# Kernel tuning notes

Hardware: AMD Instinct MI355X
Metric: run time of the kernel (lower is better)

Reference implementation:

```python
import jax, jax.numpy as jnp
import numpy as np

NUM_CLASSES = 3
NUM_ANCHORS = 3
K = 5 + NUM_CLASSES  # box(4) + obj(1) + classes


def _scale_losses(pred, boxes, labels, pos, neg):
    # pred: [B, A*K, H, W] -> [B, A*H*W, K] matching torch view/permute/view
    B, C, H, W = pred.shape
    p = pred.reshape(B, NUM_ANCHORS, K, H, W).transpose(0, 1, 3, 4, 2).reshape(B, -1, K)
    loc, obj, cls = p[..., :4], p[..., 4], p[..., 5:]
    posf = pos.astype(p.dtype)
    # BCE-with-logits, target = pos_mask: softplus(x) - t*x
    loss_obj = jnp.logaddexp(0.0, obj) - obj * posf  # [B, N]
    num_pos = pos.sum(axis=1)                         # [B] int
    num_neg = jnp.minimum(3 * num_pos, neg.sum(axis=1))
    # hard negative mining: take top-num_neg objectness losses among negatives
    masked = jnp.where(neg, loss_obj, -jnp.inf)
    order = jnp.argsort(-masked, axis=1)
    rank = jnp.argsort(order, axis=1)                 # rank 0 = largest neg loss
    sel = neg & (rank < num_neg[:, None])
    obj_per = (jnp.sum(loss_obj * posf, axis=1) +
               jnp.sum(jnp.where(sel, loss_obj, 0.0), axis=1)) / jnp.maximum(1, num_pos)
    # classification CE, mean over positive anchors
    logp = jax.nn.log_softmax(cls, axis=-1)
    ce = -jnp.take_along_axis(logp, labels[..., None].astype(jnp.int32), axis=-1)[..., 0]
    has_pos = num_pos > 0
    denom = jnp.maximum(num_pos, 1).astype(p.dtype)
    cls_per = jnp.where(has_pos, jnp.sum(ce * posf, axis=1) / denom, 0.0)
    # smooth L1 (beta=1), mean over positive anchors x 4 coords
    d = loc - boxes
    ad = jnp.abs(d)
    sl1 = jnp.where(ad < 1.0, 0.5 * d * d, ad - 0.5)
    loc_per = jnp.where(has_pos,
                        jnp.sum(sl1 * posf[..., None], axis=(1, 2)) / (denom * 4.0), 0.0)
    return obj_per.sum(), cls_per.sum(), loc_per.sum()


def _masks(key, shape):
    u = jax.random.uniform(key, shape)
    pos = u < 0.01
    neg = (~pos) & (u < 0.96)
    return pos, neg


def setup_inputs() -> dict:
    key = jax.random.key(0)
    ks = jax.random.split(key, 12)
    B = 128
    grids = [(80, 80), (40, 40), (20, 20)]
    inp = {}
    for i, (H, W) in enumerate(grids):
        N = NUM_ANCHORS * H * W
        inp[f'pred{i}'] = jax.random.normal(ks[4 * i], (B, NUM_ANCHORS * K, H, W), jnp.float32)
        inp[f'boxes{i}'] = jax.random.uniform(ks[4 * i + 1], (B, N, 4), jnp.float32)
        inp[f'labels{i}'] = jax.random.randint(ks[4 * i + 2], (B, N), 0, NUM_CLASSES, jnp.int32)
        pos, neg = _masks(ks[4 * i + 3], (B, N))
        inp[f'pos{i}'] = pos
        inp[f'neg{i}'] = neg
    return inp


def reference(pred0, pred1, pred2, boxes0, boxes1, boxes2,
              labels0, labels1, labels2, pos0, pos1, pos2, neg0, neg1, neg2):
    B = pred0.shape[0]
    preds = (pred0, pred1, pred2)
    boxes = (boxes0, boxes1, boxes2)
    labels = (labels0, labels1, labels2)
    pos = (pos0, pos1, pos2)
    neg = (neg0, neg1, neg2)
    tot_obj = tot_cls = tot_loc = 0.0
    for s in range(3):
        o, c, l = _scale_losses(preds[s], boxes[s], labels[s], pos[s], neg[s])
        tot_obj = tot_obj + o
        tot_cls = tot_cls + c
        tot_loc = tot_loc + l
    loss_obj = tot_obj / B
    loss_cls = tot_cls / B
    loss_loc = tot_loc / B
    return loss_obj + loss_cls + loss_loc, loss_obj, loss_cls, loss_loc
```

## Files before the change

kernel.cpp:

```cpp
#include <hip/hip_runtime.h>
#include <stdint.h>

#define NA   3
#define KCH  8
#define BLK  512
#define NWV  (BLK / 64)
#define NB   2048
#define QCAP 512
#define CCAP 4096
#define LKEY 0xBFA8u

#define LOG2E 1.4426950408889634f
#define LN2   0.6931471805599453f

struct ScaleParams {
  const float*   pred;
  const float*   boxes;
  const int*     labels;
  const uint8_t* pos;
  const uint8_t* neg;
  int HW;
};

__device__ __forceinline__ float fexp2(float x) { return __builtin_amdgcn_exp2f(x); }
__device__ __forceinline__ float flog2(float x) { return __builtin_amdgcn_logf(x); }

__device__ __forceinline__ float softplus_fast(float x) {
  const float t = fexp2(-fabsf(x) * LOG2E);
  return fmaxf(x, 0.f) + flog2(1.f + t) * LN2;
}

__device__ __forceinline__ float sl1f(float d) {
  float ad = fabsf(d);
  return (ad < 1.f) ? 0.5f * d * d : ad - 0.5f;
}

__device__ __forceinline__ unsigned fkey(unsigned u) {
  return (u & 0x80000000u) ? ~u : (u | 0x80000000u);
}
__device__ __forceinline__ unsigned funkey(unsigned k) {
  return (k & 0x80000000u) ? (k & 0x7FFFFFFFu) : ~k;
}
__device__ __forceinline__ float sp16(unsigned k16) {
  return softplus_fast(__uint_as_float(funkey((k16 << 16) | 0x8000u)));
}

struct __align__(16) RowShared {
  unsigned short compact[CCAP];
  unsigned hc[NB];
  float    hs[NB];
  int      queue[QCAP];
  int      sh_qn, sh_nc;
  int      iwav[NWV];
  float    fwav[NWV];
  float    fscr[NWV];
  float    wred[NWV][4];
  int      sh_dig, sh_krem;
  float    sh_sa, sh_avg;
  int      sh_flag;
  unsigned c32[32];
  float    s32[32];
};

__device__ __forceinline__ float blockSum(float v, float* scr) {
  #pragma unroll
  for (int off = 32; off > 0; off >>= 1) v += __shfl_down(v, off);
  const int lane = threadIdx.x & 63, w = threadIdx.x >> 6;
  __syncthreads();
  if (lane == 0) scr[w] = v;
  __syncthreads();
  float r = 0.f;
  #pragma unroll
  for (int i = 0; i < NWV; ++i) r += scr[i];
  return r;
}

__device__ __forceinline__ void selectDigit4(const unsigned* cb, const float* sb,
                                             int krem_in, RowShared& S) {
  const int t = threadIdx.x, lane = t & 63, w = t >> 6;
  int c_t = 0; float s_t = 0.f;
  #pragma unroll
  for (int q = 0; q < 4; ++q) { c_t += (int)cb[q]; s_t += sb[q]; }
  int ci = c_t; float si = s_t;
  #pragma unroll
  for (int off = 1; off < 64; off <<= 1) {
    const int   co = __shfl_down(ci, off);
    const float so = __shfl_down(si, off);
    if (lane + off < 64) { ci += co; si += so; }
  }
  __syncthreads();
  if (lane == 0) { S.iwav[w] = ci; S.fwav[w] = si; }
  __syncthreads();
  int ac = 0; float as = 0.f;
  #pragma unroll
  for (int w2 = 0; w2 < NWV; ++w2)
    if (w2 > w) { ac += S.iwav[w2]; as += S.fwav[w2]; }
  int   cum_c = (ci - c_t) + ac;
  float cum_s = (si - s_t) + as;
  #pragma unroll
  for (int q = 3; q >= 0; --q) {
    const int cq = (int)cb[q];
    if (cq > 0 && cum_c < krem_in && krem_in <= cum_c + cq) {
      S.sh_dig  = t * 4 + q;
      S.sh_krem = krem_in - cum_c;
      S.sh_sa   = cum_s;
    }
    cum_c += cq; cum_s += sb[q];
  }
  __syncthreads();
}

template<int HW>
__device__ void hist_low(const ScaleParams& P, int b, RowShared& S) {
  constexpr int N = 3 * HW;
  const float* predb = P.pred + (size_t)b * (NA * KCH) * HW;
  const size_t row = (size_t)b * N;
  for (int c8 = threadIdx.x * 8; c8 < N; c8 += BLK * 8) {
    const int a = (c8 >= HW) + (c8 >= 2 * HW);
    const int cell = c8 - a * HW;
    const float* po = predb + (size_t)a * KCH * HW + 4 * HW + cell;
    const float4 o0 = *(const float4*)po;
    const float4 o1 = *(const float4*)(po + 4);
    const uint2 nmv = *(const uint2*)(P.neg + row + c8);
    #pragma unroll
    for (int q = 0; q < 8; ++q) {
      const unsigned nm = ((q < 4) ? (nmv.x >> (8 * q))
                                   : (nmv.y >> (8 * (q - 4)))) & 0xFFu;
      if (nm) {
        const float obj = (q < 4) ? (&o0.x)[q] : (&o1.x)[q - 4];
        const unsigned k16 = fkey(__float_as_uint(obj)) >> 16;
        if (k16 <= LKEY) {
          atomicAdd(&S.hc[k16 >> 5], 1u);
          atomicAdd(&S.hs[k16 >> 5], sp16(k16));
        }
      }
    }
  }
}

template<int HW>
__device__ void refine_global(const ScaleParams& P, int b, int bin1,
                              unsigned lmin, RowShared& S) {
  constexpr int N = 3 * HW;
  const float* predb = P.pred + (size_t)b * (NA * KCH) * HW;
  const size_t row = (size_t)b * N;
  for (int c8 = threadIdx.x * 8; c8 < N; c8 += BLK * 8) {
    const int a = (c8 >= HW) + (c8 >= 2 * HW);
    const int cell = c8 - a * HW;
    const float* po = predb + (size_t)a * KCH * HW + 4 * HW + cell;
    const float4 o0 = *(const float4*)po;
    const float4 o1 = *(const float4*)(po + 4);
    const uint2 nmv = *(const uint2*)(P.neg + row + c8);
    #pragma unroll
    for (int q = 0; q < 8; ++q) {
      const unsigned nm = ((q < 4) ? (nmv.x >> (8 * q))
                                   : (nmv.y >> (8 * (q - 4)))) & 0xFFu;
      if (nm) {
        const float obj = (q < 4) ? (&o0.x)[q] : (&o1.x)[q - 4];
        const unsigned k16 = fkey(__float_as_uint(obj)) >> 16;
        if (k16 > lmin && (int)(k16 >> 5) == bin1) {
          atomicAdd(&S.c32[k16 & 31u], 1u);
          atomicAdd(&S.s32[k16 & 31u], sp16(k16));
        }
      }
    }
  }
}

template<int HW>
__device__ __forceinline__ void row_impl(
    const ScaleParams P, int b, float* part, RowShared& S) {
  constexpr int N = 3 * HW;
  constexpr int ITER = (N + BLK * 8 - 1) / (BLK * 8);
  const int t = threadIdx.x;

  for (int i = t; i < NB; i += BLK) { S.hc[i] = 0u; S.hs[i] = 0.f; }
  if (t == 0) { S.sh_qn = 0; S.sh_nc = 0; }
  __syncthreads();

  const float* predb = P.pred + (size_t)b * (NA * KCH) * HW;
  const size_t row = (size_t)b * N;
  float nneg = 0.f;

  float4 o0[ITER], o1[ITER];
  uint2  pmv[ITER], nmv[ITER];
  #pragma unroll
  for (int it = 0; it < ITER; ++it) {
    const int c8 = it * (BLK * 8) + t * 8;
    if (c8 < N) {
      const int a = (c8 >= HW) + (c8 >= 2 * HW);
      const int cell = c8 - a * HW;
      const float* po = predb + (size_t)a * KCH * HW + 4 * HW + cell;
      o0[it]  = *(const float4*)po;
      o1[it]  = *(const float4*)(po + 4);
      pmv[it] = *(const uint2*)(P.pos + row + c8);
      nmv[it] = *(const uint2*)(P.neg + row + c8);
    }
  }

  #pragma unroll
  for (int it = 0; it < ITER; ++it) {
    const int c8 = it * (BLK * 8) + t * 8;
    if (c8 < N) {
      const unsigned long long nm64 =
          ((unsigned long long)nmv[it].y << 32) | nmv[it].x;
      nneg += (float)__popcll(nm64);
      #pragma unroll
      for (int q = 0; q < 8; ++q) {
        const unsigned nm = ((q < 4) ? (nmv[it].x >> (8 * q))
                                     : (nmv[it].y >> (8 * (q - 4)))) & 0xFFu;
        const unsigned pm = ((q < 4) ? (pmv[it].x >> (8 * q))
                                     : (pmv[it].y >> (8 * (q - 4)))) & 0xFFu;
        if (nm) {
          const float obj = (q < 4) ? (&o0[it].x)[q] : (&o1[it].x)[q - 4];
          const unsigned k16 = fkey(__float_as_uint(obj)) >> 16;
          if (k16 > LKEY) {
            const int ci = atomicAdd(&S.sh_nc, 1);
            if (ci < CCAP) S.compact[ci] = (unsigned short)k16;
            atomicAdd(&S.hc[k16 >> 5], 1u);
            atomicAdd(&S.hs[k16 >> 5], sp16(k16));
          }
        }
        if (pm) {
          const int idx = atomicAdd(&S.sh_qn, 1);
          if (idx < QCAP) S.queue[idx] = c8 + q;
        }
      }
    }
  }
  __syncthreads();
  const int npos = S.sh_qn;
  const int nc   = S.sh_nc;
  const int qn = min(npos, QCAP);

  float posobj = 0.f, ce = 0.f, loc = 0.f;
  for (int i = t; i < qn; i += BLK) {
    const int j = S.queue[i];
    const int a = (j >= HW) + (j >= 2 * HW);
    const int cell = j - a * HW;
    const float* pa = predb + (size_t)a * KCH * HW;
    posobj += softplus_fast(-pa[4 * HW + cell]);
    const float c0f = pa[5 * HW + cell];
    const float c1f = pa[6 * HW + cell];
    const float c2f = pa[7 * HW + cell];
    const float m = fmaxf(fmaxf(c0f, c1f), c2f);
    const float e = fexp2((c0f - m) * LOG2E) + fexp2((c1f - m) * LOG2E)
                  + fexp2((c2f - m) * LOG2E);
    const float lse = m + flog2(e) * LN2;
    const int lab = P.labels[row + j];
    ce += lse - ((lab == 0) ? c0f : (lab == 1) ? c1f : c2f);
    const float4 bx = *(const float4*)(P.boxes + (size_t)(row + j) * 4);
    loc += sl1f(pa[0 * HW + cell] - bx.x) + sl1f(pa[1 * HW + cell] - bx.y)
         + sl1f(pa[2 * HW + cell] - bx.z) + sl1f(pa[3 * HW + cell] - bx.w);
  }

  {
    float v[4] = {nneg, posobj, ce, loc};
    #pragma unroll
    for (int i = 0; i < 4; ++i) {
      #pragma unroll
      for (int off = 32; off > 0; off >>= 1) v[i] += __shfl_down(v[i], off);
    }
    const int lane = t & 63, w = t >> 6;
    __syncthreads();
    if (lane == 0) {
      #pragma unroll
      for (int i = 0; i < 4; ++i) S.wred[w][i] = v[i];
    }
    __syncthreads();
  }
  float red[4];
  #pragma unroll
  for (int i = 0; i < 4; ++i) {
    float acc = 0.f;
    #pragma unroll
    for (int w2 = 0; w2 < NWV; ++w2) acc += S.wred[w2][i];
    red[i] = acc;
  }
  const float t_po = red[1], t_ce = red[2], t_lc = red[3];
  const int k = min(3 * npos, (int)red[0]);

  float sel = 0.f;
  if (k > 0) {
    unsigned lmin = LKEY;
    const bool fell = (nc < k);
    if (fell) {
      hist_low<HW>(P, b, S);
      __syncthreads();
      lmin = 0u;
    }

    unsigned cb[4]; float sb[4];
    #pragma unroll
    for (int q = 0; q < 4; ++q) { cb[q] = S.hc[4*t+q]; sb[q] = S.hs[4*t+q]; }
    selectDigit4(cb, sb, k, S);
    const int bin1 = S.sh_dig; const int krem1 = S.sh_krem;
    const float sa1 = S.sh_sa;

    if (t < 32) { S.c32[t] = 0u; S.s32[t] = 0.f; }
    __syncthreads();

    if (!fell && nc <= CCAP) {
      for (int i = t; i < nc; i += BLK) {
        const unsigned k16 = S.compact[i];
        if ((int)(k16 >> 5) == bin1) {
          atomicAdd(&S.c32[k16 & 31u], 1u);
          atomicAdd(&S.s32[k16 & 31u], sp16(k16));
        }
      }
    } else {
      refine_global<HW>(P, b, bin1, lmin, S);
    }
    __syncthreads();

    if (t < 64) {
      const int cc = (t < 32) ? (int)S.c32[t] : 0;
      const float ss = (t < 32) ? S.s32[t] : 0.f;
      int ci = cc; float si = ss;
      #pragma unroll
      for (int off = 1; off < 64; off <<= 1) {
        const int   co = __shfl_down(ci, off);
        const float so = __shfl_down(si, off);
        if ((t & 63) + off < 64) { ci += co; si += so; }
      }
      const int   above_c = ci - cc;
      const float above_s = si - ss;
      if (t < 32 && cc > 0 && above_c < krem1 && krem1 <= above_c + cc) {
        S.sh_krem = krem1 - above_c;
        S.sh_sa   = sa1 + above_s;
        S.sh_avg  = ss / (float)cc;
      }
    }
    __syncthreads();
    sel = S.sh_sa + (float)S.sh_krem * S.sh_avg;
  }

  if (t == 0) {
    const float denom = (float)max(npos, 1);
    part[0] = (t_po + sel) / denom;
    part[1] = (npos > 0) ? t_ce / denom : 0.f;
    part[2] = (npos > 0) ? t_lc / (denom * 4.f) : 0.f;
  }
}

__global__ void k_zero(unsigned* done) {
  if (threadIdx.x == 0) *done = 0u;
}

__global__ __launch_bounds__(BLK) void k_row(
    ScaleParams p0, ScaleParams p1, ScaleParams p2,
    int B, int R, float invB, float* g_part, unsigned* done, float* out) {
  __shared__ RowShared S;
  const int r = blockIdx.x;
  const int s = (r >= B) + (r >= 2 * B);
  const int b = r - s * B;
  float* part = g_part + (size_t)r * 4;
  if (s == 0)      row_impl<6400>(p0, b, part, S);
  else if (s == 1) row_impl<1600>(p1, b, part, S);
  else             row_impl<400>(p2, b, part, S);

  if (threadIdx.x == 0) {
    __threadfence();
    const unsigned old = atomicAdd(done, 1u);
    S.sh_flag = (old == (unsigned)(R - 1)) ? 1 : 0;
  }
  __syncthreads();
  if (S.sh_flag) {
    __threadfence();
    const int t = threadIdx.x;
    float o = 0.f, c = 0.f, l = 0.f;
    for (int i = t; i < R; i += BLK) {
      o += g_part[i * 4 + 0];
      c += g_part[i * 4 + 1];
      l += g_part[i * 4 + 2];
    }
    o = blockSum(o, S.fscr);
    c = blockSum(c, S.fscr);
    l = blockSum(l, S.fscr);
    if (t == 0) {
      out[0] = (o + c + l) * invB;
      out[1] = o * invB;
      out[2] = c * invB;
      out[3] = l * invB;
    }
  }
}

extern "C" void kernel_launch(void* const* d_in, const int* in_sizes, int n_in,
                              void* d_out, int out_size, void* d_ws, size_t ws_size,
                              hipStream_t stream) {
  (void)n_in; (void)out_size; (void)ws_size;

  const int HW0 = 80 * 80, HW1 = 40 * 40, HW2 = 20 * 20;
  const int B = in_sizes[0] / (NA * KCH * HW0);
  const int R = 3 * B;
  const float invB = 1.f / (float)B;

  ScaleParams p0{(const float*)d_in[0],  (const float*)d_in[1],
                 (const int*)d_in[2],    (const uint8_t*)d_in[3],
                 (const uint8_t*)d_in[4], HW0};
  ScaleParams p1{(const float*)d_in[5],  (const float*)d_in[6],
                 (const int*)d_in[7],    (const uint8_t*)d_in[8],
                 (const uint8_t*)d_in[9], HW1};
  ScaleParams p2{(const float*)d_in[10], (const float*)d_in[11],
                 (const int*)d_in[12],   (const uint8_t*)d_in[13],
                 (const uint8_t*)d_in[14], HW2};

  float* out = (float*)d_out;
  unsigned* done = (unsigned*)d_ws;
  float* g_part = (float*)((char*)d_ws + 256);

  k_zero<<<1, 64, 0, stream>>>(done);
  k_row<<<R, BLK, 0, stream>>>(p0, p1, p2, B, R, invB, g_part, done, out);
}
```

Baseline: 28.74 us.

## Split large-scale rows across two blocks and merge candidates via global handoff

```diff
diff --git a/kernel.cpp b/kernel.cpp
--- a/kernel.cpp
+++ b/kernel.cpp
@@ -7,7 +7,8 @@
 #define NWV  (BLK / 64)
 #define NB   2048
 #define QCAP 512
-#define CCAP 4096
+#define HCAP 3072
+#define CCAP 6400
 #define LKEY 0xBFA8u
 
 #define LOG2E 1.4426950408889634f
@@ -45,19 +46,25 @@
   return softplus_fast(__uint_as_float(funkey((k16 << 16) | 0x8000u)));
 }
 
+__device__ __forceinline__ unsigned aload(const unsigned* p) {
+  return __hip_atomic_load(p, __ATOMIC_RELAXED, __HIP_MEMORY_SCOPE_AGENT);
+}
+__device__ __forceinline__ void astore(unsigned* p, unsigned v) {
+  __hip_atomic_store(p, v, __ATOMIC_RELAXED, __HIP_MEMORY_SCOPE_AGENT);
+}
+
 struct __align__(16) RowShared {
   unsigned short compact[CCAP];
   unsigned hc[NB];
-  float    hs[NB];
   int      queue[QCAP];
   int      sh_qn, sh_nc;
   int      iwav[NWV];
-  float    fwav[NWV];
   float    fscr[NWV];
   float    wred[NWV][4];
   int      sh_dig, sh_krem;
   float    sh_sa, sh_avg;
   int      sh_flag;
+  unsigned sh_sib[8];
   unsigned c32[32];
   float    s32[32];
 };
@@ -75,47 +82,126 @@
   return r;
 }
 
-__device__ __forceinline__ void selectDigit4(const unsigned* cb, const float* sb,
-                                             int krem_in, RowShared& S) {
+__device__ __forceinline__ void selectBin1(const unsigned* cb, int krem_in,
+                                           RowShared& S) {
   const int t = threadIdx.x, lane = t & 63, w = t >> 6;
-  int c_t = 0; float s_t = 0.f;
-  #pragma unroll
-  for (int q = 0; q < 4; ++q) { c_t += (int)cb[q]; s_t += sb[q]; }
-  int ci = c_t; float si = s_t;
+  const int c_t = (int)(cb[0] + cb[1] + cb[2] + cb[3]);
+  int ci = c_t;
   #pragma unroll
   for (int off = 1; off < 64; off <<= 1) {
-    const int   co = __shfl_down(ci, off);
-    const float so = __shfl_down(si, off);
-    if (lane + off < 64) { ci += co; si += so; }
-  }
-  __syncthreads();
-  if (lane == 0) { S.iwav[w] = ci; S.fwav[w] = si; }
-  __syncthreads();
-  int ac = 0; float as = 0.f;
-  #pragma unroll
-  for (int w2 = 0; w2 < NWV; ++w2)
-    if (w2 > w) { ac += S.iwav[w2]; as += S.fwav[w2]; }
-  int   cum_c = (ci - c_t) + ac;
-  float cum_s = (si - s_t) + as;
+    const int co = __shfl_down(ci, off);
+    if (lane + off < 64) ci += co;
+  }
+  __syncthreads();
+  if (lane == 0) S.iwav[w] = ci;
+  __syncthreads();
+  int ac = 0;
+  #pragma unroll
+  for (int w2 = 0; w2 < NWV; ++w2) if (w2 > w) ac += S.iwav[w2];
+  int cum_c = (ci - c_t) + ac;
   #pragma unroll
   for (int q = 3; q >= 0; --q) {
     const int cq = (int)cb[q];
     if (cq > 0 && cum_c < krem_in && krem_in <= cum_c + cq) {
       S.sh_dig  = t * 4 + q;
       S.sh_krem = krem_in - cum_c;
-      S.sh_sa   = cum_s;
-    }
-    cum_c += cq; cum_s += sb[q];
-  }
-  __syncthreads();
+    }
+    cum_c += cq;
+  }
+  __syncthreads();
+}
+
+__device__ __forceinline__ float stage2_sel(int krem1, float sa1, RowShared& S) {
+  const int t = threadIdx.x;
+  if (t < 64) {
+    const int cc = (t < 32) ? (int)S.c32[t] : 0;
+    const float ss = (t < 32) ? S.s32[t] : 0.f;
+    int ci = cc; float si = ss;
+    #pragma unroll
+    for (int off = 1; off < 64; off <<= 1) {
+      const int   co = __shfl_down(ci, off);
+      const float so = __shfl_down(si, off);
+      if ((t & 63) + off < 64) { ci += co; si += so; }
+    }
+    const int   above_c = ci - cc;
+    const float above_s = si - ss;
+    if (t < 32 && cc > 0 && above_c < krem1 && krem1 <= above_c + cc) {
+      S.sh_krem = krem1 - above_c;
+      S.sh_sa   = sa1 + above_s;
+      S.sh_avg  = ss / (float)cc;
+    }
+  }
+  __syncthreads();
+  return S.sh_sa + (float)S.sh_krem * S.sh_avg;
+}
+
+__device__ float select_compact(int m, int k, RowShared& S) {
+  const int t = threadIdx.x;
+  for (int i = t; i < NB; i += BLK) S.hc[i] = 0u;
+  __syncthreads();
+  for (int i = t; i < m; i += BLK) {
+    const unsigned k16 = S.compact[i];
+    if (k16) atomicAdd(&S.hc[k16 >> 5], 1u);
+  }
+  __syncthreads();
+  unsigned cb[4];
+  #pragma unroll
+  for (int q = 0; q < 4; ++q) cb[q] = S.hc[4 * t + q];
+  selectBin1(cb, k, S);
+  const int bin1 = S.sh_dig, krem1 = S.sh_krem;
+  if (t < 32) { S.c32[t] = 0u; S.s32[t] = 0.f; }
+  __syncthreads();
+  float sgt = 0.f;
+  for (int i = t; i < m; i += BLK) {
+    const unsigned k16 = S.compact[i];
+    if (!k16) continue;
+    const int kb = (int)(k16 >> 5);
+    if (kb > bin1) sgt += sp16(k16);
+    else if (kb == bin1) {
+      atomicAdd(&S.c32[k16 & 31u], 1u);
+      atomicAdd(&S.s32[k16 & 31u], sp16(k16));
+    }
+  }
+  __syncthreads();
+  const float t_sgt = blockSum(sgt, S.fscr);
+  return stage2_sel(krem1, t_sgt, S);
 }
 
 template<int HW>
-__device__ void hist_low(const ScaleParams& P, int b, RowShared& S) {
+__device__ float select_full(const ScaleParams& P, int b, int k, RowShared& S) {
   constexpr int N = 3 * HW;
+  const int t = threadIdx.x;
   const float* predb = P.pred + (size_t)b * (NA * KCH) * HW;
   const size_t row = (size_t)b * N;
-  for (int c8 = threadIdx.x * 8; c8 < N; c8 += BLK * 8) {
+  for (int i = t; i < NB; i += BLK) S.hc[i] = 0u;
+  __syncthreads();
+  for (int c8 = t * 8; c8 < N; c8 += BLK * 8) {
+    const int a = (c8 >= HW) + (c8 >= 2 * HW);
+    const int cell = c8 - a * HW;
+    const float* po = predb + (size_t)a * KCH * HW + 4 * HW + cell;
+    const float4 o0 = *(const float4*)po;
+    const float4 o1 = *(const float4*)(po + 4);
+    const uint2 nmv = *(const uint2*)(P.neg + row + c8);
+    #pragma unroll
+    for (int q = 0; q < 8; ++q) {
+      const unsigned nm = ((q < 4) ? (nmv.x >> (8 * q))
+                                   : (nmv.y >> (8 * (q - 4)))) & 0xFFu;
+      if (nm) {
+        const float obj = (q < 4) ? (&o0.x)[q] : (&o1.x)[q - 4];
+        atomicAdd(&S.hc[(fkey(__float_as_uint(obj)) >> 16) >> 5], 1u);
+      }
+    }
+  }
+  __syncthreads();
+  unsigned cb[4];
+  #pragma unroll
+  for (int q = 0; q < 4; ++q) cb[q] = S.hc[4 * t + q];
+  selectBin1(cb, k, S);
+  const int bin1 = S.sh_dig, krem1 = S.sh_krem;
+  if (t < 32) { S.c32[t] = 0u; S.s32[t] = 0.f; }
+  __syncthreads();
+  float sgt = 0.f;
+  for (int c8 = t * 8; c8 < N; c8 += BLK * 8) {
     const int a = (c8 >= HW) + (c8 >= 2 * HW);
     const int cell = c8 - a * HW;
     const float* po = predb + (size_t)a * KCH * HW + 4 * HW + cell;
@@ -129,65 +215,38 @@
       if (nm) {
         const float obj = (q < 4) ? (&o0.x)[q] : (&o1.x)[q - 4];
         const unsigned k16 = fkey(__float_as_uint(obj)) >> 16;
-        if (k16 <= LKEY) {
-          atomicAdd(&S.hc[k16 >> 5], 1u);
-          atomicAdd(&S.hs[k16 >> 5], sp16(k16));
-        }
-      }
-    }
-  }
-}
-
-template<int HW>
-__device__ void refine_global(const ScaleParams& P, int b, int bin1,
-                              unsigned lmin, RowShared& S) {
-  constexpr int N = 3 * HW;
-  const float* predb = P.pred + (size_t)b * (NA * KCH) * HW;
-  const size_t row = (size_t)b * N;
-  for (int c8 = threadIdx.x * 8; c8 < N; c8 += BLK * 8) {
-    const int a = (c8 >= HW) + (c8 >= 2 * HW);
-    const int cell = c8 - a * HW;
-    const float* po = predb + (size_t)a * KCH * HW + 4 * HW + cell;
-    const float4 o0 = *(const float4*)po;
-    const float4 o1 = *(const float4*)(po + 4);
-    const uint2 nmv = *(const uint2*)(P.neg + row + c8);
-    #pragma unroll
-    for (int q = 0; q < 8; ++q) {
-      const unsigned nm = ((q < 4) ? (nmv.x >> (8 * q))
-                                   : (nmv.y >> (8 * (q - 4)))) & 0xFFu;
-      if (nm) {
-        const float obj = (q < 4) ? (&o0.x)[q] : (&o1.x)[q - 4];
-        const unsigned k16 = fkey(__float_as_uint(obj)) >> 16;
-        if (k16 > lmin && (int)(k16 >> 5) == bin1) {
+        const int kb = (int)(k16 >> 5);
+        if (kb > bin1) sgt += sp16(k16);
+        else if (kb == bin1) {
           atomicAdd(&S.c32[k16 & 31u], 1u);
           atomicAdd(&S.s32[k16 & 31u], sp16(k16));
         }
       }
     }
   }
-}
-
-template<int HW>
-__device__ __forceinline__ void row_impl(
-    const ScaleParams P, int b, float* part, RowShared& S) {
-  constexpr int N = 3 * HW;
-  constexpr int ITER = (N + BLK * 8 - 1) / (BLK * 8);
+  __syncthreads();
+  const float t_sgt = blockSum(sgt, S.fscr);
+  return stage2_sel(krem1, t_sgt, S);
+}
+
+template<int HW, int NLOC>
+__device__ __forceinline__ int scan_range(
+    const ScaleParams& P, int b, int c0, RowShared& S, float red[4]) {
+  constexpr int ITER = (NLOC + BLK * 8 - 1) / (BLK * 8);
   const int t = threadIdx.x;
-
-  for (int i = t; i < NB; i += BLK) { S.hc[i] = 0u; S.hs[i] = 0.f; }
   if (t == 0) { S.sh_qn = 0; S.sh_nc = 0; }
   __syncthreads();
 
   const float* predb = P.pred + (size_t)b * (NA * KCH) * HW;
-  const size_t row = (size_t)b * N;
+  const size_t row = (size_t)b * (3 * HW);
   float nneg = 0.f;
 
   float4 o0[ITER], o1[ITER];
   uint2  pmv[ITER], nmv[ITER];
   #pragma unroll
   for (int it = 0; it < ITER; ++it) {
-    const int c8 = it * (BLK * 8) + t * 8;
-    if (c8 < N) {
+    const int c8 = c0 + it * (BLK * 8) + t * 8;
+    if (c8 < c0 + NLOC) {
       const int a = (c8 >= HW) + (c8 >= 2 * HW);
       const int cell = c8 - a * HW;
       const float* po = predb + (size_t)a * KCH * HW + 4 * HW + cell;
@@ -197,40 +256,45 @@
       nmv[it] = *(const uint2*)(P.neg + row + c8);
     }
   }
-
   #pragma unroll
   for (int it = 0; it < ITER; ++it) {
-    const int c8 = it * (BLK * 8) + t * 8;
-    if (c8 < N) {
+    const int c8 = c0 + it * (BLK * 8) + t * 8;
+    if (c8 < c0 + NLOC) {
       const unsigned long long nm64 =
           ((unsigned long long)nmv[it].y << 32) | nmv[it].x;
       nneg += (float)__popcll(nm64);
+      unsigned k16s[8], cmask = 0u;
       #pragma unroll
       for (int q = 0; q < 8; ++q) {
         const unsigned nm = ((q < 4) ? (nmv[it].x >> (8 * q))
                                      : (nmv[it].y >> (8 * (q - 4)))) & 0xFFu;
         const unsigned pm = ((q < 4) ? (pmv[it].x >> (8 * q))
                                      : (pmv[it].y >> (8 * (q - 4)))) & 0xFFu;
+        unsigned k16 = 0u;
         if (nm) {
-          const float obj = (q < 4) ? (&o0[it].x)[q] : (&o1[it].x)[q - 4];
-          const unsigned k16 = fkey(__float_as_uint(obj)) >> 16;
-          if (k16 > LKEY) {
-            const int ci = atomicAdd(&S.sh_nc, 1);
-            if (ci < CCAP) S.compact[ci] = (unsigned short)k16;
-            atomicAdd(&S.hc[k16 >> 5], 1u);
-            atomicAdd(&S.hs[k16 >> 5], sp16(k16));
-          }
+          k16 = fkey(__float_as_uint((q < 4) ? (&o0[it].x)[q]
+                                             : (&o1[it].x)[q - 4])) >> 16;
+          if (k16 > LKEY) cmask |= (1u << q);
         }
+        k16s[q] = k16;
         if (pm) {
           const int idx = atomicAdd(&S.sh_qn, 1);
           if (idx < QCAP) S.queue[idx] = c8 + q;
         }
       }
+      if (cmask) {
+        const int ci = atomicAdd(&S.sh_nc, (int)__popc(cmask));
+        #pragma unroll
+        for (int q = 0; q < 8; ++q)
+          if ((cmask >> q) & 1u) {
+            const int p = ci + (int)__popc(cmask & ((1u << q) - 1u));
+            if (p < CCAP) S.compact[p] = (unsigned short)k16s[q];
+          }
+      }
     }
   }
   __syncthreads();
   const int npos = S.sh_qn;
-  const int nc   = S.sh_nc;
   const int qn = min(npos, QCAP);
 
   float posobj = 0.f, ce = 0.f, loc = 0.f;
@@ -269,7 +333,6 @@
     }
     __syncthreads();
   }
-  float red[4];
   #pragma unroll
   for (int i = 0; i < 4; ++i) {
     float acc = 0.f;
@@ -277,87 +340,134 @@
     for (int w2 = 0; w2 < NWV; ++w2) acc += S.wred[w2][i];
     red[i] = acc;
   }
-  const float t_po = red[1], t_ce = red[2], t_lc = red[3];
+  return npos;
+}
+
+template<int HW>
+__device__ __forceinline__ void row_whole(const ScaleParams& P, int b,
+                                          float* part, RowShared& S) {
+  float red[4];
+  const int npos = scan_range<HW, 3 * HW>(P, b, 0, S, red);
+  const int nc = S.sh_nc;
   const int k = min(3 * npos, (int)red[0]);
-
   float sel = 0.f;
   if (k > 0) {
-    unsigned lmin = LKEY;
-    const bool fell = (nc < k);
-    if (fell) {
-      hist_low<HW>(P, b, S);
-      __syncthreads();
-      lmin = 0u;
-    }
-
-    unsigned cb[4]; float sb[4];
-    #pragma unroll
-    for (int q = 0; q < 4; ++q) { cb[q] = S.hc[4*t+q]; sb[q] = S.hs[4*t+q]; }
-    selectDigit4(cb, sb, k, S);
-    const int bin1 = S.sh_dig; const int krem1 = S.sh_krem;
-    const float sa1 = S.sh_sa;
-
-    if (t < 32) { S.c32[t] = 0u; S.s32[t] = 0.f; }
-    __syncthreads();
-
-    if (!fell && nc <= CCAP) {
-      for (int i = t; i < nc; i += BLK) {
-        const unsigned k16 = S.compact[i];
-        if ((int)(k16 >> 5) == bin1) {
-          atomicAdd(&S.c32[k16 & 31u], 1u);
-          atomicAdd(&S.s32[k16 & 31u], sp16(k16));
-        }
-      }
-    } else {
-      refine_global<HW>(P, b, bin1, lmin, S);
-    }
-    __syncthreads();
-
-    if (t < 64) {
-      const int cc = (t < 32) ? (int)S.c32[t] : 0;
-      const float ss = (t < 32) ? S.s32[t] : 0.f;
-      int ci = cc; float si = ss;
-      #pragma unroll
-      for (int off = 1; off < 64; off <<= 1) {
-        const int   co = __shfl_down(ci, off);
-        const float so = __shfl_down(si, off);
-        if ((t & 63) + off < 64) { ci += co; si += so; }
-      }
-      const int   above_c = ci - cc;
-      const float above_s = si - ss;
-      if (t < 32 && cc > 0 && above_c < krem1 && krem1 <= above_c + cc) {
-        S.sh_krem = krem1 - above_c;
-        S.sh_sa   = sa1 + above_s;
-        S.sh_avg  = ss / (float)cc;
-      }
-    }
-    __syncthreads();
-    sel = S.sh_sa + (float)S.sh_krem * S.sh_avg;
-  }
-
+    if (nc <= CCAP && nc >= k) sel = select_compact(min(nc, CCAP), k, S);
+    else                       sel = select_full<HW>(P, b, k, S);
+  }
+  if (threadIdx.x == 0) {
+    const float denom = (float)max(npos, 1);
+    part[0] = (red[1] + sel) / denom;
+    part[1] = (npos > 0) ? red[2] / denom : 0.f;
+    part[2] = (npos > 0) ? red[3] / (denom * 4.f) : 0.f;
+  }
+}
+
+__device__ bool row_s0_half(
+    const ScaleParams& p0, int b, int half,
+    unsigned* g_cmp, unsigned* g_sc, unsigned* g_tick,
+    float* part, RowShared& S) {
+  constexpr int HW = 6400, NLOC = 9600;
+  float red[4];
+  const int npos = scan_range<HW, NLOC>(p0, b, half * NLOC, S, red);
+  const int nc = S.sh_nc;
+  const int t = threadIdx.x;
+  const int ncs = min(nc, HCAP);
+
+  if (t == 0 && (ncs & 1)) S.compact[ncs] = 0;
+  __syncthreads();
+  const size_t hid = (size_t)b * 2 + half;
+  unsigned* cmp = g_cmp + hid * (HCAP / 2);
+  for (int i = t; i < (ncs + 1) / 2; i += BLK)
+    astore(&cmp[i], (unsigned)S.compact[2 * i] |
+                    ((unsigned)S.compact[2 * i + 1] << 16));
   if (t == 0) {
-    const float denom = (float)max(npos, 1);
-    part[0] = (t_po + sel) / denom;
-    part[1] = (npos > 0) ? t_ce / denom : 0.f;
-    part[2] = (npos > 0) ? t_lc / (denom * 4.f) : 0.f;
-  }
-}
-
-__global__ void k_zero(unsigned* done) {
+    unsigned* sc = g_sc + hid * 8;
+    astore(&sc[0], (unsigned)npos);
+    astore(&sc[1], __float_as_uint(red[0]));
+    astore(&sc[2], __float_as_uint(red[1]));
+    astore(&sc[3], __float_as_uint(red[2]));
+    astore(&sc[4], __float_as_uint(red[3]));
+    astore(&sc[5], (unsigned)nc);
+  }
+  __syncthreads();
+  if (t == 0) {
+    const unsigned old = __hip_atomic_fetch_add(
+        &g_tick[b], 1u, __ATOMIC_ACQ_REL, __HIP_MEMORY_SCOPE_AGENT);
+    S.sh_flag = (old == 1u) ? 1 : 0;
+  }
+  __syncthreads();
+  if (!S.sh_flag) return false;
+
+  const size_t oid = (size_t)b * 2 + (half ^ 1);
+  if (t < 6) S.sh_sib[t] = aload(g_sc + oid * 8 + t);
+  __syncthreads();
+  const int   npos2 = (int)S.sh_sib[0];
+  const float nneg2 = __uint_as_float(S.sh_sib[1]);
+  const float po2   = __uint_as_float(S.sh_sib[2]);
+  const float ce2   = __uint_as_float(S.sh_sib[3]);
+  const float lc2   = __uint_as_float(S.sh_sib[4]);
+  const int   nc2   = (int)S.sh_sib[5];
+  const int   nc2s  = min(nc2, HCAP);
+  const unsigned* cmp2 = g_cmp + oid * (HCAP / 2);
+  const int base = ncs;
+  for (int i = t; i < (nc2s + 1) / 2; i += BLK) {
+    const unsigned w = aload(&cmp2[i]);
+    const int p = base + 2 * i;
+    if (p < CCAP)     S.compact[p]     = (unsigned short)(w & 0xFFFFu);
+    if (p + 1 < CCAP) S.compact[p + 1] = (unsigned short)(w >> 16);
+  }
+  __syncthreads();
+
+  const int   npos_t = npos + npos2;
+  const float nneg_t = red[0] + nneg2;
+  const float po_t   = red[1] + po2;
+  const float ce_t   = red[2] + ce2;
+  const float lc_t   = red[3] + lc2;
+  const int   abv_t  = nc + nc2;
+  const int   m      = min(base + 2 * ((nc2s + 1) / 2), CCAP);
+
+  const int k = min(3 * npos_t, (int)nneg_t);
+  float sel = 0.f;
+  if (k > 0) {
+    if (nc <= HCAP && nc2 <= HCAP && abv_t >= k)
+      sel = select_compact(m, k, S);
+    else
+      sel = select_full<HW>(p0, b, k, S);
+  }
+  if (t == 0) {
+    const float denom = (float)max(npos_t, 1);
+    part[0] = (po_t + sel) / denom;
+    part[1] = (npos_t > 0) ? ce_t / denom : 0.f;
+    part[2] = (npos_t > 0) ? lc_t / (denom * 4.f) : 0.f;
+  }
+  return true;
+}
+
+__global__ void k_zero(unsigned* g_tick, int B, unsigned* done) {
+  for (int i = threadIdx.x; i < B; i += blockDim.x) g_tick[i] = 0u;
   if (threadIdx.x == 0) *done = 0u;
 }
 
 __global__ __launch_bounds__(BLK) void k_row(
-    ScaleParams p0, ScaleParams p1, ScaleParams p2,
-    int B, int R, float invB, float* g_part, unsigned* done, float* out) {
+    ScaleParams p0, ScaleParams p1, ScaleParams p2, int B, int R, float invB,
+    unsigned* g_cmp, unsigned* g_sc, unsigned* g_tick,
+    float* g_part, unsigned* done, float* out) {
   __shared__ RowShared S;
-  const int r = blockIdx.x;
-  const int s = (r >= B) + (r >= 2 * B);
-  const int b = r - s * B;
-  float* part = g_part + (size_t)r * 4;
-  if (s == 0)      row_impl<6400>(p0, b, part, S);
-  else if (s == 1) row_impl<1600>(p1, b, part, S);
-  else             row_impl<400>(p2, b, part, S);
+  const int bid = blockIdx.x;
+  bool emit = true;
+  if (bid < 2 * B) {
+    const int b = bid >> 1, half = bid & 1;
+    emit = row_s0_half(p0, b, half, g_cmp, g_sc, g_tick,
+                       g_part + (size_t)b * 4, S);
+  } else if (bid < 3 * B) {
+    const int b = bid - 2 * B;
+    row_whole<1600>(p1, b, g_part + (size_t)(B + b) * 4, S);
+  } else {
+    const int b = bid - 3 * B;
+    row_whole<400>(p2, b, g_part + (size_t)(2 * B + b) * 4, S);
+  }
+  if (!emit) return;
 
   if (threadIdx.x == 0) {
     __threadfence();
@@ -407,9 +517,15 @@
                  (const uint8_t*)d_in[14], HW2};
 
   float* out = (float*)d_out;
-  unsigned* done = (unsigned*)d_ws;
-  float* g_part = (float*)((char*)d_ws + 256);
-
-  k_zero<<<1, 64, 0, stream>>>(done);
-  k_row<<<R, BLK, 0, stream>>>(p0, p1, p2, B, R, invB, g_part, done, out);
-}
+
+  char* w = (char*)d_ws;
+  unsigned* done   = (unsigned*)w;  w += 256;
+  unsigned* g_tick = (unsigned*)w;  w += (((size_t)B * 4 + 255) & ~255ull);
+  float*    g_part = (float*)w;     w += (((size_t)R * 16 + 255) & ~255ull);
+  unsigned* g_sc   = (unsigned*)w;  w += (((size_t)B * 2 * 8 * 4 + 255) & ~255ull);
+  unsigned* g_cmp  = (unsigned*)w;  w += (size_t)B * 2 * (HCAP / 2) * 4;
+
+  k_zero<<<1, 256, 0, stream>>>(g_tick, B, done);
+  k_row<<<4 * B, BLK, 0, stream>>>(p0, p1, p2, B, R, invB,
+                                   g_cmp, g_sc, g_tick, g_part, done, out);
+}
```

Result: slower. 34.02 us (+18.4%).

## Build selection histogram from compacted keys after scan, drop sum histogram

Applied to the files above, without the earlier changes.

```diff
diff --git a/kernel.cpp b/kernel.cpp
--- a/kernel.cpp
+++ b/kernel.cpp
@@ -48,11 +48,9 @@
 struct __align__(16) RowShared {
   unsigned short compact[CCAP];
   unsigned hc[NB];
-  float    hs[NB];
   int      queue[QCAP];
   int      sh_qn, sh_nc;
   int      iwav[NWV];
-  float    fwav[NWV];
   float    fscr[NWV];
   float    wred[NWV][4];
   int      sh_dig, sh_krem;
@@ -75,47 +73,123 @@
   return r;
 }
 
-__device__ __forceinline__ void selectDigit4(const unsigned* cb, const float* sb,
-                                             int krem_in, RowShared& S) {
+__device__ __forceinline__ void selectBin1(const unsigned* cb, int krem_in,
+                                           RowShared& S) {
   const int t = threadIdx.x, lane = t & 63, w = t >> 6;
-  int c_t = 0; float s_t = 0.f;
-  #pragma unroll
-  for (int q = 0; q < 4; ++q) { c_t += (int)cb[q]; s_t += sb[q]; }
-  int ci = c_t; float si = s_t;
+  const int c_t = (int)(cb[0] + cb[1] + cb[2] + cb[3]);
+  int ci = c_t;
   #pragma unroll
   for (int off = 1; off < 64; off <<= 1) {
-    const int   co = __shfl_down(ci, off);
-    const float so = __shfl_down(si, off);
-    if (lane + off < 64) { ci += co; si += so; }
-  }
-  __syncthreads();
-  if (lane == 0) { S.iwav[w] = ci; S.fwav[w] = si; }
-  __syncthreads();
-  int ac = 0; float as = 0.f;
-  #pragma unroll
-  for (int w2 = 0; w2 < NWV; ++w2)
-    if (w2 > w) { ac += S.iwav[w2]; as += S.fwav[w2]; }
-  int   cum_c = (ci - c_t) + ac;
-  float cum_s = (si - s_t) + as;
+    const int co = __shfl_down(ci, off);
+    if (lane + off < 64) ci += co;
+  }
+  __syncthreads();
+  if (lane == 0) S.iwav[w] = ci;
+  __syncthreads();
+  int ac = 0;
+  #pragma unroll
+  for (int w2 = 0; w2 < NWV; ++w2) if (w2 > w) ac += S.iwav[w2];
+  int cum_c = (ci - c_t) + ac;
   #pragma unroll
   for (int q = 3; q >= 0; --q) {
     const int cq = (int)cb[q];
     if (cq > 0 && cum_c < krem_in && krem_in <= cum_c + cq) {
       S.sh_dig  = t * 4 + q;
       S.sh_krem = krem_in - cum_c;
-      S.sh_sa   = cum_s;
-    }
-    cum_c += cq; cum_s += sb[q];
-  }
-  __syncthreads();
+    }
+    cum_c += cq;
+  }
+  __syncthreads();
+}
+
+__device__ __forceinline__ float stage2_sel(int krem1, float sa1, RowShared& S) {
+  const int t = threadIdx.x;
+  if (t < 64) {
+    const int cc = (t < 32) ? (int)S.c32[t] : 0;
+    const float ss = (t < 32) ? S.s32[t] : 0.f;
+    int ci = cc; float si = ss;
+    #pragma unroll
+    for (int off = 1; off < 64; off <<= 1) {
+      const int   co = __shfl_down(ci, off);
+      const float so = __shfl_down(si, off);
+      if ((t & 63) + off < 64) { ci += co; si += so; }
+    }
+    const int   above_c = ci - cc;
+    const float above_s = si - ss;
+    if (t < 32 && cc > 0 && above_c < krem1 && krem1 <= above_c + cc) {
+      S.sh_krem = krem1 - above_c;
+      S.sh_sa   = sa1 + above_s;
+      S.sh_avg  = ss / (float)cc;
+    }
+  }
+  __syncthreads();
+  return S.sh_sa + (float)S.sh_krem * S.sh_avg;
+}
+
+__device__ float select_compact(int m, int k, RowShared& S) {
+  const int t = threadIdx.x;
+  for (int i = t; i < NB; i += BLK) S.hc[i] = 0u;
+  __syncthreads();
+  for (int i = t; i < m; i += BLK)
+    atomicAdd(&S.hc[S.compact[i] >> 5], 1u);
+  __syncthreads();
+  unsigned cb[4];
+  #pragma unroll
+  for (int q = 0; q < 4; ++q) cb[q] = S.hc[4 * t + q];
+  selectBin1(cb, k, S);
+  const int bin1 = S.sh_dig, krem1 = S.sh_krem;
+  if (t < 32) { S.c32[t] = 0u; S.s32[t] = 0.f; }
+  __syncthreads();
+  float sgt = 0.f;
+  for (int i = t; i < m; i += BLK) {
+    const unsigned k16 = S.compact[i];
+    const int kb = (int)(k16 >> 5);
+    if (kb > bin1) sgt += sp16(k16);
+    else if (kb == bin1) {
+      atomicAdd(&S.c32[k16 & 31u], 1u);
+      atomicAdd(&S.s32[k16 & 31u], sp16(k16));
+    }
+  }
+  __syncthreads();
+  const float t_sgt = blockSum(sgt, S.fscr);
+  return stage2_sel(krem1, t_sgt, S);
 }
 
 template<int HW>
-__device__ void hist_low(const ScaleParams& P, int b, RowShared& S) {
+__device__ float select_full(const ScaleParams& P, int b, int k, RowShared& S) {
   constexpr int N = 3 * HW;
+  const int t = threadIdx.x;
   const float* predb = P.pred + (size_t)b * (NA * KCH) * HW;
   const size_t row = (size_t)b * N;
-  for (int c8 = threadIdx.x * 8; c8 < N; c8 += BLK * 8) {
+  for (int i = t; i < NB; i += BLK) S.hc[i] = 0u;
+  __syncthreads();
+  for (int c8 = t * 8; c8 < N; c8 += BLK * 8) {
+    const int a = (c8 >= HW) + (c8 >= 2 * HW);
+    const int cell = c8 - a * HW;
+    const float* po = predb + (size_t)a * KCH * HW + 4 * HW + cell;
+    const float4 o0 = *(const float4*)po;
+    const float4 o1 = *(const float4*)(po + 4);
+    const uint2 nmv = *(const uint2*)(P.neg + row + c8);
+    #pragma unroll
+    for (int q = 0; q < 8; ++q) {
+      const unsigned nm = ((q < 4) ? (nmv.x >> (8 * q))
+                                   : (nmv.y >> (8 * (q - 4)))) & 0xFFu;
+      if (nm) {
+        const float obj = (q < 4) ? (&o0.x)[q] : (&o1.x)[q - 4];
+        atomicAdd(&S.hc[(fkey(__float_as_uint(obj)) >> 16) >> 5], 1u);
+      }
+    }
+  }
+  __syncthreads();
+  unsigned cb[4];
+  #pragma unroll
+  for (int q = 0; q < 4; ++q) cb[q] = S.hc[4 * t + q];
+  selectBin1(cb, k, S);
+  const int bin1 = S.sh_dig, krem1 = S.sh_krem;
+  if (t < 32) { S.c32[t] = 0u; S.s32[t] = 0.f; }
+  __syncthreads();
+  float sgt = 0.f;
+  for (int c8 = t * 8; c8 < N; c8 += BLK * 8) {
     const int a = (c8 >= HW) + (c8 >= 2 * HW);
     const int cell = c8 - a * HW;
     const float* po = predb + (size_t)a * KCH * HW + 4 * HW + cell;
@@ -129,52 +203,26 @@
       if (nm) {
         const float obj = (q < 4) ? (&o0.x)[q] : (&o1.x)[q - 4];
         const unsigned k16 = fkey(__float_as_uint(obj)) >> 16;
-        if (k16 <= LKEY) {
-          atomicAdd(&S.hc[k16 >> 5], 1u);
-          atomicAdd(&S.hs[k16 >> 5], sp16(k16));
-        }
-      }
-    }
-  }
-}
-
-template<int HW>
-__device__ void refine_global(const ScaleParams& P, int b, int bin1,
-                              unsigned lmin, RowShared& S) {
-  constexpr int N = 3 * HW;
-  const float* predb = P.pred + (size_t)b * (NA * KCH) * HW;
-  const size_t row = (size_t)b * N;
-  for (int c8 = threadIdx.x * 8; c8 < N; c8 += BLK * 8) {
-    const int a = (c8 >= HW) + (c8 >= 2 * HW);
-    const int cell = c8 - a * HW;
-    const float* po = predb + (size_t)a * KCH * HW + 4 * HW + cell;
-    const float4 o0 = *(const float4*)po;
-    const float4 o1 = *(const float4*)(po + 4);
-    const uint2 nmv = *(const uint2*)(P.neg + row + c8);
-    #pragma unroll
-    for (int q = 0; q < 8; ++q) {
-      const unsigned nm = ((q < 4) ? (nmv.x >> (8 * q))
-                                   : (nmv.y >> (8 * (q - 4)))) & 0xFFu;
-      if (nm) {
-        const float obj = (q < 4) ? (&o0.x)[q] : (&o1.x)[q - 4];
-        const unsigned k16 = fkey(__float_as_uint(obj)) >> 16;
-        if (k16 > lmin && (int)(k16 >> 5) == bin1) {
+        const int kb = (int)(k16 >> 5);
+        if (kb > bin1) sgt += sp16(k16);
+        else if (kb == bin1) {
           atomicAdd(&S.c32[k16 & 31u], 1u);
           atomicAdd(&S.s32[k16 & 31u], sp16(k16));
         }
       }
     }
   }
+  __syncthreads();
+  const float t_sgt = blockSum(sgt, S.fscr);
+  return stage2_sel(krem1, t_sgt, S);
 }
 
 template<int HW>
-__device__ __forceinline__ void row_impl(
+__device__ __forceinline__ void row_whole(
     const ScaleParams P, int b, float* part, RowShared& S) {
   constexpr int N = 3 * HW;
   constexpr int ITER = (N + BLK * 8 - 1) / (BLK * 8);
   const int t = threadIdx.x;
-
-  for (int i = t; i < NB; i += BLK) { S.hc[i] = 0u; S.hs[i] = 0.f; }
   if (t == 0) { S.sh_qn = 0; S.sh_nc = 0; }
   __syncthreads();
 
@@ -205,26 +253,33 @@
       const unsigned long long nm64 =
           ((unsigned long long)nmv[it].y << 32) | nmv[it].x;
       nneg += (float)__popcll(nm64);
+      unsigned k16s[8], cmask = 0u;
       #pragma unroll
       for (int q = 0; q < 8; ++q) {
         const unsigned nm = ((q < 4) ? (nmv[it].x >> (8 * q))
                                      : (nmv[it].y >> (8 * (q - 4)))) & 0xFFu;
         const unsigned pm = ((q < 4) ? (pmv[it].x >> (8 * q))
                                      : (pmv[it].y >> (8 * (q - 4)))) & 0xFFu;
+        unsigned k16 = 0u;
         if (nm) {
-          const float obj = (q < 4) ? (&o0[it].x)[q] : (&o1[it].x)[q - 4];
-          const unsigned k16 = fkey(__float_as_uint(obj)) >> 16;
-          if (k16 > LKEY) {
-            const int ci = atomicAdd(&S.sh_nc, 1);
-            if (ci < CCAP) S.compact[ci] = (unsigned short)k16;
-            atomicAdd(&S.hc[k16 >> 5], 1u);
-            atomicAdd(&S.hs[k16 >> 5], sp16(k16));
-          }
+          k16 = fkey(__float_as_uint((q < 4) ? (&o0[it].x)[q]
+                                             : (&o1[it].x)[q - 4])) >> 16;
+          if (k16 > LKEY) cmask |= (1u << q);
         }
+        k16s[q] = k16;
         if (pm) {
           const int idx = atomicAdd(&S.sh_qn, 1);
           if (idx < QCAP) S.queue[idx] = c8 + q;
         }
+      }
+      if (cmask) {
+        const int ci = atomicAdd(&S.sh_nc, (int)__popc(cmask));
+        #pragma unroll
+        for (int q = 0; q < 8; ++q)
+          if ((cmask >> q) & 1u) {
+            const int p = ci + (int)__popc(cmask & ((1u << q) - 1u));
+            if (p < CCAP) S.compact[p] = (unsigned short)k16s[q];
+          }
       }
     }
   }
@@ -277,69 +332,19 @@
     for (int w2 = 0; w2 < NWV; ++w2) acc += S.wred[w2][i];
     red[i] = acc;
   }
-  const float t_po = red[1], t_ce = red[2], t_lc = red[3];
   const int k = min(3 * npos, (int)red[0]);
 
   float sel = 0.f;
   if (k > 0) {
-    unsigned lmin = LKEY;
-    const bool fell = (nc < k);
-    if (fell) {
-      hist_low<HW>(P, b, S);
-      __syncthreads();
-      lmin = 0u;
-    }
-
-    unsigned cb[4]; float sb[4];
-    #pragma unroll
-    for (int q = 0; q < 4; ++q) { cb[q] = S.hc[4*t+q]; sb[q] = S.hs[4*t+q]; }
-    selectDigit4(cb, sb, k, S);
-    const int bin1 = S.sh_dig; const int krem1 = S.sh_krem;
-    const float sa1 = S.sh_sa;
-
-    if (t < 32) { S.c32[t] = 0u; S.s32[t] = 0.f; }
-    __syncthreads();
-
-    if (!fell && nc <= CCAP) {
-      for (int i = t; i < nc; i += BLK) {
-        const unsigned k16 = S.compact[i];
-        if ((int)(k16 >> 5) == bin1) {
-          atomicAdd(&S.c32[k16 & 31u], 1u);
-          atomicAdd(&S.s32[k16 & 31u], sp16(k16));
-        }
-      }
-    } else {
-      refine_global<HW>(P, b, bin1, lmin, S);
-    }
-    __syncthreads();
-
-    if (t < 64) {
-      const int cc = (t < 32) ? (int)S.c32[t] : 0;
-      const float ss = (t < 32) ? S.s32[t] : 0.f;
-      int ci = cc; float si = ss;
-      #pragma unroll
-      for (int off = 1; off < 64; off <<= 1) {
-        const int   co = __shfl_down(ci, off);
-        const float so = __shfl_down(si, off);
-        if ((t & 63) + off < 64) { ci += co; si += so; }
-      }
-      const int   above_c = ci - cc;
-      const float above_s = si - ss;
-      if (t < 32 && cc > 0 && above_c < krem1 && krem1 <= above_c + cc) {
-        S.sh_krem = krem1 - above_c;
-        S.sh_sa   = sa1 + above_s;
-        S.sh_avg  = ss / (float)cc;
-      }
-    }
-    __syncthreads();
-    sel = S.sh_sa + (float)S.sh_krem * S.sh_avg;
+    if (nc <= CCAP && nc >= k) sel = select_compact(nc, k, S);
+    else                       sel = select_full<HW>(P, b, k, S);
   }
 
   if (t == 0) {
     const float denom = (float)max(npos, 1);
-    part[0] = (t_po + sel) / denom;
-    part[1] = (npos > 0) ? t_ce / denom : 0.f;
-    part[2] = (npos > 0) ? t_lc / (denom * 4.f) : 0.f;
+    part[0] = (red[1] + sel) / denom;
+    part[1] = (npos > 0) ? red[2] / denom : 0.f;
+    part[2] = (npos > 0) ? red[3] / (denom * 4.f) : 0.f;
   }
 }
 
@@ -355,9 +360,9 @@
   const int s = (r >= B) + (r >= 2 * B);
   const int b = r - s * B;
   float* part = g_part + (size_t)r * 4;
-  if (s == 0)      row_impl<6400>(p0, b, part, S);
-  else if (s == 1) row_impl<1600>(p1, b, part, S);
-  else             row_impl<400>(p2, b, part, S);
+  if (s == 0)      row_whole<6400>(p0, b, part, S);
+  else if (s == 1) row_whole<1600>(p1, b, part, S);
+  else             row_whole<400>(p2, b, part, S);
 
   if (threadIdx.x == 0) {
     __threadfence();
```

Measured after the change: 30.78 us. 7.1% more time.
